# Kernel optimization log

Measured on AMD Instinct MI355X. Metric: run time of the kernel, lower is better.

The kernel has to match this reference:

```python
import jax, jax.numpy as jnp
import numpy as np

B, S, D, H, F = 2, 2048, 2048, 16, 6144
HD = D // H  # 128
EPS = 1e-5
NEG = -1e9


def layernorm(x, g, b):
    m = jnp.mean(x, axis=-1, keepdims=True)
    v = jnp.var(x, axis=-1, keepdims=True)
    return (x - m) * jax.lax.rsqrt(v + EPS) * g + b


def setup_inputs() -> dict:
    key = jax.random.key(0)
    ks = jax.random.split(key, 16)
    w = 0.02
    hidden_states = jax.random.normal(ks[0], (B, S, D), jnp.float32)
    # additive causal mask [B,1,S,S]
    causal = jnp.tril(jnp.ones((S, S), jnp.bool_))
    attention_mask = jnp.broadcast_to(jnp.where(causal, 0.0, NEG).astype(jnp.float32)[None, None], (B, 1, S, S))
    # ALiBi position bias [H,S,S]
    slopes = 2.0 ** (-8.0 * (jnp.arange(1, H + 1, dtype=jnp.float32)) / H)
    rel = (jnp.arange(S)[None, :] - jnp.arange(S)[:, None]).astype(jnp.float32)  # j - i (<=0 causal)
    position_bias = slopes[:, None, None] * rel[None]
    params = dict(
        ln1_g=jnp.ones((D,), jnp.float32), ln1_b=jnp.zeros((D,), jnp.float32),
        w_qkv=jax.random.normal(ks[1], (D, 3 * D), jnp.float32) * w,
        b_qkv=jnp.zeros((3 * D,), jnp.float32),
        w_o=jax.random.normal(ks[2], (D, D), jnp.float32) * w,
        b_o=jnp.zeros((D,), jnp.float32),
        ln2_g=jnp.ones((D,), jnp.float32), ln2_b=jnp.zeros((D,), jnp.float32),
        w_fc=jax.random.normal(ks[3], (D, F), jnp.float32) * w,
        b_fc=jnp.zeros((F,), jnp.float32),
        w_fc2=jax.random.normal(ks[4], (D, F), jnp.float32) * w,
        b_fc2=jnp.zeros((F,), jnp.float32),
        w_proj=jax.random.normal(ks[5], (F, D), jnp.float32) * w,
        b_proj=jnp.zeros((D,), jnp.float32),
    )
    return dict(hidden_states=hidden_states, attention_mask=attention_mask,
                position_bias=position_bias, **params)


def reference(hidden_states, attention_mask, position_bias,
              ln1_g, ln1_b, w_qkv, b_qkv, w_o, b_o,
              ln2_g, ln2_b, w_fc, b_fc, w_fc2, b_fc2, w_proj, b_proj):
    residual = hidden_states
    h = layernorm(hidden_states, ln1_g, ln1_b)
    qkv = h @ w_qkv + b_qkv  # [B,S,3D]
    q, k, v = jnp.split(qkv, 3, axis=-1)
    # split heads -> [B,H,S,HD]
    def heads(t):
        return t.reshape(B, S, H, HD).transpose(0, 2, 1, 3)
    q, k, v = heads(q), heads(k), heads(v)
    # muP scaling: attn_scale_power=1.0 -> divide by head_dim
    scores = jnp.einsum('bhqd,bhkd->bhqk', q, k) / jnp.float32(HD)
    scores = scores + attention_mask + position_bias[None]
    probs = jax.nn.softmax(scores, axis=-1)
    ctx = jnp.einsum('bhqk,bhkd->bhqd', probs, v)
    ctx = ctx.transpose(0, 2, 1, 3).reshape(B, S, D)
    attn_out = ctx @ w_o + b_o
    hidden = attn_out + residual
    # SwiGLU MLP
    residual = hidden
    h2 = layernorm(hidden, ln2_g, ln2_b)
    gate = h2 @ w_fc2 + b_fc2
    up = h2 @ w_fc + b_fc
    mlp = (up * jax.nn.silu(gate)) @ w_proj + b_proj
    return mlp + residual
```

## Files before the change

kernel.cpp:

```cpp
#include <hip/hip_runtime.h>
#include <hip/hip_bf16.h>
#include <math.h>

#define DI __device__ __forceinline__

typedef __bf16 bf16x8 __attribute__((ext_vector_type(8)));
typedef float f32x4 __attribute__((ext_vector_type(4)));
typedef short s16x8 __attribute__((ext_vector_type(8)));

DI unsigned short f2bf(float f) {
  unsigned int u = __builtin_bit_cast(unsigned int, f);
  unsigned int r = (u + 0x7fffu + ((u >> 16) & 1u)) >> 16;
  return (unsigned short)r;
}
DI float bf2f(unsigned short h) {
  unsigned int u = ((unsigned int)h) << 16;
  return __builtin_bit_cast(float, u);
}

DI void gload16(const void* g, void* l) {
  __builtin_amdgcn_global_load_lds(
      (const __attribute__((address_space(1))) void*)g,
      (__attribute__((address_space(3))) void*)l, 16, 0, 0);
}

DI unsigned ldsoff(const void* p) {
  return (unsigned)(size_t)(const __attribute__((address_space(3))) void*)p;
}

template <int OFF>
DI bf16x8 ds128(unsigned base) {
  bf16x8 r;
  asm volatile("ds_read_b128 %0, %1 offset:%2" : "=v"(r) : "v"(base), "i"(OFF));
  return r;
}
template <int N>
DI void lgkm() {
  asm volatile("s_waitcnt lgkmcnt(%0)" ::"i"(N));
  __builtin_amdgcn_sched_barrier(0);
}
template <int N>
DI void vmc() {
  asm volatile("s_waitcnt vmcnt(%0)" ::"i"(N));
  __builtin_amdgcn_sched_barrier(0);
}

DI void xcd_map(int BN, int& m0, int& n0) {
  const int nx = gridDim.x;
  int orig = blockIdx.y * nx + blockIdx.x;
  int xcd = orig & 7, k = orig >> 3;
  int xm = xcd >> 2, xn = xcd & 3;
  int nband = nx >> 2;
  m0 = (xm * 8 + (k & 7)) * 256;
  n0 = (xn * nband + (k >> 3)) * BN;
}

__global__ __launch_bounds__(256)
void transpose_cast_f32(const float* __restrict__ in, unsigned short* __restrict__ out,
                        int R, int C) {
  __shared__ unsigned int t[64 * 65];
  const int r0 = blockIdx.y * 64, c0 = blockIdx.x * 64;
  const int tid = threadIdx.x;
#pragma unroll
  for (int p = 0; p < 4; ++p) {
    int e = p * 1024 + tid * 4;
    int r = e >> 6, c = e & 63;
    float4 v = *(const float4*)(in + (size_t)(r0 + r) * C + c0 + c);
    t[r * 65 + c + 0] = f2bf(v.x);
    t[r * 65 + c + 1] = f2bf(v.y);
    t[r * 65 + c + 2] = f2bf(v.z);
    t[r * 65 + c + 3] = f2bf(v.w);
  }
  __syncthreads();
  const int oc = tid >> 2, ch = tid & 3;
  alignas(16) unsigned short vals[16];
#pragma unroll
  for (int j = 0; j < 16; ++j) vals[j] = (unsigned short)t[(ch * 16 + j) * 65 + oc];
  size_t ob = (size_t)(c0 + oc) * R + r0 + ch * 16;
  *(s16x8*)(out + ob) = *(const s16x8*)(vals);
  *(s16x8*)(out + ob + 8) = *(const s16x8*)(vals + 8);
}

__global__ __launch_bounds__(256)
void transpose_v(const unsigned short* __restrict__ qkv, unsigned short* __restrict__ vT) {
  __shared__ unsigned int t[64 * 65];
  const int s0 = blockIdx.x * 64, d0 = blockIdx.y * 64, bh = blockIdx.z;
  const int b = bh >> 4, h = bh & 15;
  const int tid = threadIdx.x;
#pragma unroll
  for (int p = 0; p < 2; ++p) {
    int id = p * 256 + tid;
    int r = id >> 3, c = (id & 7) * 8;
    s16x8 v = *(const s16x8*)(qkv + (size_t)(b * 2048 + s0 + r) * 6144 + 4096 + h * 128 + d0 + c);
#pragma unroll
    for (int j = 0; j < 8; ++j) t[r * 65 + c + j] = (unsigned short)((const unsigned short*)&v)[j];
  }
  __syncthreads();
  const int oc = tid >> 2, ch = tid & 3;
  alignas(16) unsigned short vals[16];
#pragma unroll
  for (int j = 0; j < 16; ++j) vals[j] = (unsigned short)t[(ch * 16 + j) * 65 + oc];
  size_t ob = (size_t)(bh * 128 + d0 + oc) * 2048 + s0 + ch * 16;
  *(s16x8*)(vT + ob) = *(const s16x8*)(vals);
  *(s16x8*)(vT + ob + 8) = *(const s16x8*)(vals + 8);
}

__global__ __launch_bounds__(256)
void ln_kernel(const float* __restrict__ x, const float* __restrict__ g,
               const float* __restrict__ bi, unsigned short* __restrict__ y) {
  __shared__ float red[8];
  const int row = blockIdx.x, tid = threadIdx.x;
  const float* xp = x + (size_t)row * 2048 + tid * 8;
  float4 v0 = *(const float4*)xp;
  float4 v1 = *(const float4*)(xp + 4);
  float v[8] = {v0.x, v0.y, v0.z, v0.w, v1.x, v1.y, v1.z, v1.w};
  float s = 0.f;
#pragma unroll
  for (int j = 0; j < 8; ++j) s += v[j];
#pragma unroll
  for (int d = 1; d < 64; d <<= 1) s += __shfl_xor(s, d);
  if ((tid & 63) == 0) red[tid >> 6] = s;
  __syncthreads();
  float mean = (red[0] + red[1] + red[2] + red[3]) * (1.f / 2048.f);
  float dd[8], sq = 0.f;
#pragma unroll
  for (int j = 0; j < 8; ++j) { dd[j] = v[j] - mean; sq += dd[j] * dd[j]; }
#pragma unroll
  for (int d = 1; d < 64; d <<= 1) sq += __shfl_xor(sq, d);
  if ((tid & 63) == 0) red[4 + (tid >> 6)] = sq;
  __syncthreads();
  float var = (red[4] + red[5] + red[6] + red[7]) * (1.f / 2048.f);
  float rs = rsqrtf(var + 1e-5f);
  float4 g0 = *(const float4*)(g + tid * 8), g1 = *(const float4*)(g + tid * 8 + 4);
  float4 b0 = *(const float4*)(bi + tid * 8), b1 = *(const float4*)(bi + tid * 8 + 4);
  float gg[8] = {g0.x, g0.y, g0.z, g0.w, g1.x, g1.y, g1.z, g1.w};
  float bb[8] = {b0.x, b0.y, b0.z, b0.w, b1.x, b1.y, b1.z, b1.w};
  alignas(16) unsigned short o[8];
#pragma unroll
  for (int j = 0; j < 8; ++j) o[j] = f2bf(dd[j] * rs * gg[j] + bb[j]);
  *(s16x8*)(y + (size_t)row * 2048 + tid * 8) = *(const s16x8*)o;
}

DI void stage_half(const unsigned short* __restrict__ G, int ld, int rbase, int kt,
                   int h, unsigned short* dst, int tid) {
#pragma unroll
  for (int i = 0; i < 2; ++i) {
    int id = i * 512 + tid;
    int rl = id >> 3, sl = id & 7;
    int ss = sl ^ (rl & 7);
    gload16(G + (size_t)(rbase + h * 128 + rl) * ld + kt + ss * 8,
            (char*)dst + h * 16384 + id * 16);
  }
}

template <int MODE>
__global__ __launch_bounds__(512, 2)
void gemm256(const unsigned short* __restrict__ A, int lda,
             const unsigned short* __restrict__ B,
             const float* __restrict__ bias,
             const void* __restrict__ resg,
             void* __restrict__ out, int ldc, int K) {
  __shared__ alignas(16) unsigned short As[2][256 * 64];
  __shared__ alignas(16) unsigned short Bs[2][256 * 64];

  const int tid = threadIdx.x;
  const int l = tid & 63, w = tid >> 6;
  const int wr = w >> 2, wc = w & 3;
  const int lr = l & 15, lg = l >> 4;

  int m0, n0;
  xcd_map(256, m0, n0);

  const int NT = K >> 6;

  f32x4 acc[8][4];
  const f32x4 z4 = {0.f, 0.f, 0.f, 0.f};
#pragma unroll
  for (int i = 0; i < 8; ++i)
#pragma unroll
    for (int j = 0; j < 4; ++j) acc[i][j] = z4;

  const int s7 = lr & 7;
  const unsigned swz0 = (unsigned)((lg ^ s7) << 4);
  const unsigned swz1 = (unsigned)(((4 | lg) ^ s7) << 4);
  const unsigned rA = (unsigned)((wr * 128 + lr) * 128);
  const unsigned rB = (unsigned)((wc * 64 + lr) * 128);
  const unsigned aA0 = ldsoff(&As[0][0]) + rA + swz0;
  const unsigned aA1 = ldsoff(&As[0][0]) + rA + swz1;
  const unsigned bA0 = ldsoff(&Bs[0][0]) + rB + swz0;
  const unsigned bA1 = ldsoff(&Bs[0][0]) + rB + swz1;

  stage_half(A, lda, m0, 0, 0, As[0], tid);
  stage_half(A, lda, m0, 0, 1, As[0], tid);
  stage_half(B, K, n0, 0, 0, Bs[0], tid);
  stage_half(B, K, n0, 0, 1, Bs[0], tid);
  if (NT > 1) {
    stage_half(B, K, n0, 64, 0, Bs[1], tid);
    stage_half(B, K, n0, 64, 1, Bs[1], tid);
    stage_half(A, lda, m0, 64, 0, As[1], tid);
    asm volatile("s_waitcnt vmcnt(6)" ::: "memory");
  } else {
    asm volatile("s_waitcnt vmcnt(0)" ::: "memory");
  }
  __builtin_amdgcn_s_barrier();

  for (int t = 0; t < NT; ++t) {
    const unsigned co = (unsigned)((t & 1) * 32768);
    const unsigned a0b = aA0 + co, a1b = aA1 + co;
    const unsigned b0b = bA0 + co, b1b = bA1 + co;
    bf16x8 a0[4][2], a1[4][2], bfr[4][2];

#pragma unroll
    for (int i = 0; i < 4; ++i) {
      a0[i][0] = ds128<0 * 2048>(a0b + i * 2048);
      a0[i][1] = ds128<0 * 2048>(a1b + i * 2048);
    }
#pragma unroll
    for (int j = 0; j < 2; ++j) {
      bfr[j][0] = ds128<0>(b0b + j * 2048);
      bfr[j][1] = ds128<0>(b1b + j * 2048);
    }
    if (t + 1 < NT) stage_half(A, lda, m0, (t + 1) * 64, 1, As[(t & 1) ^ 1], tid);
#pragma unroll
    for (int j = 2; j < 4; ++j) {
      bfr[j][0] = ds128<0>(b0b + j * 2048);
      bfr[j][1] = ds128<0>(b1b + j * 2048);
    }
    lgkm<4>();
    __builtin_amdgcn_s_setprio(1);
#pragma unroll
    for (int i = 0; i < 4; ++i)
#pragma unroll
      for (int j = 0; j < 2; ++j)
#pragma unroll
        for (int kk = 0; kk < 2; ++kk)
          acc[i][j] = __builtin_amdgcn_mfma_f32_16x16x32_bf16(a0[i][kk], bfr[j][kk], acc[i][j], 0, 0, 0);
    __builtin_amdgcn_s_setprio(0);
    __builtin_amdgcn_s_barrier();

#pragma unroll
    for (int i = 0; i < 4; ++i) {
      a1[i][0] = ds128<8192>(a0b + i * 2048);
      a1[i][1] = ds128<8192>(a1b + i * 2048);
    }
    lgkm<8>();
    __builtin_amdgcn_s_setprio(1);
#pragma unroll
    for (int i = 0; i < 4; ++i)
#pragma unroll
      for (int j = 2; j < 4; ++j)
#pragma unroll
        for (int kk = 0; kk < 2; ++kk)
          acc[i][j] = __builtin_amdgcn_mfma_f32_16x16x32_bf16(a0[i][kk], bfr[j][kk], acc[i][j], 0, 0, 0);
    __builtin_amdgcn_s_setprio(0);
    __builtin_amdgcn_s_barrier();

    if (t + 2 < NT) stage_half(B, K, n0, (t + 2) * 64, 0, Bs[t & 1], tid);
    lgkm<0>();
    __builtin_amdgcn_s_setprio(1);
#pragma unroll
    for (int i = 0; i < 4; ++i)
#pragma unroll
      for (int j = 0; j < 2; ++j)
#pragma unroll
        for (int kk = 0; kk < 2; ++kk)
          acc[i + 4][j] = __builtin_amdgcn_mfma_f32_16x16x32_bf16(a1[i][kk], bfr[j][kk], acc[i + 4][j], 0, 0, 0);
    __builtin_amdgcn_s_setprio(0);
    __builtin_amdgcn_s_barrier();

    if (t + 2 < NT) {
      stage_half(B, K, n0, (t + 2) * 64, 1, Bs[t & 1], tid);
      stage_half(A, lda, m0, (t + 2) * 64, 0, As[t & 1], tid);
    }
    __builtin_amdgcn_s_setprio(1);
#pragma unroll
    for (int i = 0; i < 4; ++i)
#pragma unroll
      for (int j = 2; j < 4; ++j)
#pragma unroll
        for (int kk = 0; kk < 2; ++kk)
          acc[i + 4][j] = __builtin_amdgcn_mfma_f32_16x16x32_bf16(a1[i][kk], bfr[j][kk], acc[i + 4][j], 0, 0, 0);
    __builtin_amdgcn_s_setprio(0);
    if (t + 2 < NT) { vmc<6>(); } else { vmc<0>(); }
    __builtin_amdgcn_s_barrier();
  }

#pragma unroll
  for (int i = 0; i < 8; ++i) {
    int r0 = m0 + wr * 128 + i * 16 + lg * 4;
#pragma unroll
    for (int j = 0; j < 4; ++j) {
      int col = n0 + wc * 64 + j * 16 + lr;
      float bb = bias[col];
#pragma unroll
      for (int q = 0; q < 4; ++q) {
        size_t off = (size_t)(r0 + q) * ldc + col;
        float v = acc[i][j][q] + bb;
        if (MODE == 0) {
          ((unsigned short*)out)[off] = f2bf(v);
        } else {
          ((float*)out)[off] = v + ((const float*)resg)[off];
        }
      }
    }
  }
}

template <int MODE, bool DUAL>
__global__ __launch_bounds__(512, 2)
void gemm_n128(const unsigned short* __restrict__ A, int lda,
               const unsigned short* __restrict__ B0,
               const unsigned short* __restrict__ B1,
               const float* __restrict__ bias0, const float* __restrict__ bias1,
               const void* __restrict__ resg,
               void* __restrict__ out, int ldc, int K) {
  __shared__ alignas(16) unsigned short As[2][256 * 64];
  __shared__ alignas(16) unsigned short Bs0[2][128 * 64];

  const int tid = threadIdx.x;
  const int l = tid & 63, w = tid >> 6;
  const int wr = w >> 2, wc = w & 3;
  const int lr = l & 15, lg = l >> 4;

  int m0, n0;
  xcd_map(128, m0, n0);

  const int NT = K >> 6;

  f32x4 acc0[8][2];
  const f32x4 z4 = {0.f, 0.f, 0.f, 0.f};
#pragma unroll
  for (int i = 0; i < 8; ++i)
#pragma unroll
    for (int j = 0; j < 2; ++j) acc0[i][j] = z4;

  const int s7 = lr & 7;
  const unsigned swz0 = (unsigned)((lg ^ s7) << 4);
  const unsigned swz1 = (unsigned)(((4 | lg) ^ s7) << 4);
  const unsigned rA = (unsigned)((wr * 128 + lr) * 128);
  const unsigned rB = (unsigned)((wc * 32 + lr) * 128);
  const unsigned aA0 = ldsoff(&As[0][0]) + rA + swz0;
  const unsigned aA1 = ldsoff(&As[0][0]) + rA + swz1;
  const unsigned bA0 = ldsoff(&Bs0[0][0]) + rB + swz0;
  const unsigned bA1 = ldsoff(&Bs0[0][0]) + rB + swz1;

  stage_half(A, lda, m0, 0, 0, As[0], tid);
  stage_half(A, lda, m0, 0, 1, As[0], tid);
  stage_half(B0, K, n0, 0, 0, Bs0[0], tid);
  if (NT > 1) {
    stage_half(B0, K, n0, 64, 0, Bs0[1], tid);
    stage_half(A, lda, m0, 64, 0, As[1], tid);
    asm volatile("s_waitcnt vmcnt(4)" ::: "memory");
  } else {
    asm volatile("s_waitcnt vmcnt(0)" ::: "memory");
  }
  __builtin_amdgcn_s_barrier();

  for (int t = 0; t < NT; ++t) {
    const int cur = t & 1;
    const unsigned ca = aA0 + (unsigned)(cur * 32768);
    const unsigned ca1 = aA1 + (unsigned)(cur * 32768);
    const unsigned cb = bA0 + (unsigned)(cur * 16384);
    const unsigned cb1 = bA1 + (unsigned)(cur * 16384);
    bf16x8 a0[4][2], a1[4][2], b0f[2][2];

#pragma unroll
    for (int i = 0; i < 4; ++i) {
      a0[i][0] = ds128<0>(ca + i * 2048);
      a0[i][1] = ds128<0>(ca1 + i * 2048);
    }
#pragma unroll
    for (int j = 0; j < 2; ++j) {
      b0f[j][0] = ds128<0>(cb + j * 2048);
      b0f[j][1] = ds128<0>(cb1 + j * 2048);
    }
    if (t + 1 < NT) stage_half(A, lda, m0, (t + 1) * 64, 1, As[cur ^ 1], tid);
#pragma unroll
    for (int i = 0; i < 4; ++i) {
      a1[i][0] = ds128<8192>(ca + i * 2048);
      a1[i][1] = ds128<8192>(ca1 + i * 2048);
    }
    lgkm<8>();
    __builtin_amdgcn_s_setprio(1);
#pragma unroll
    for (int i = 0; i < 4; ++i)
#pragma unroll
      for (int j = 0; j < 2; ++j)
#pragma unroll
        for (int kk = 0; kk < 2; ++kk)
          acc0[i][j] = __builtin_amdgcn_mfma_f32_16x16x32_bf16(a0[i][kk], b0f[j][kk], acc0[i][j], 0, 0, 0);
    __builtin_amdgcn_s_setprio(0);
    __builtin_amdgcn_s_barrier();

    if (t + 2 < NT) stage_half(B0, K, n0, (t + 2) * 64, 0, Bs0[cur], tid);
    lgkm<0>();
    if (t + 2 < NT) stage_half(A, lda, m0, (t + 2) * 64, 0, As[cur], tid);
    __builtin_amdgcn_s_setprio(1);
#pragma unroll
    for (int i = 0; i < 4; ++i)
#pragma unroll
      for (int j = 0; j < 2; ++j)
#pragma unroll
        for (int kk = 0; kk < 2; ++kk)
          acc0[i + 4][j] = __builtin_amdgcn_mfma_f32_16x16x32_bf16(a1[i][kk], b0f[j][kk], acc0[i + 4][j], 0, 0, 0);
    __builtin_amdgcn_s_setprio(0);
    if (t + 2 < NT) { vmc<4>(); } else { vmc<0>(); }
    __builtin_amdgcn_s_barrier();
  }

#pragma unroll
  for (int i = 0; i < 8; ++i) {
    int r0 = m0 + wr * 128 + i * 16 + lg * 4;
#pragma unroll
    for (int j = 0; j < 2; ++j) {
      int col = n0 + wc * 32 + j * 16 + lr;
      float bb0 = bias0[col];
#pragma unroll
      for (int q = 0; q < 4; ++q) {
        size_t off = (size_t)(r0 + q) * ldc + col;
        float v = acc0[i][j][q] + bb0;
        ((float*)out)[off] = v + ((const float*)resg)[off];
      }
    }
  }
}

DI void mmq(f32x4 (&acc)[8][2], int io, const bf16x8 (&af)[4][2], const bf16x8 (&bf)[2][2]) {
#pragma unroll
  for (int kk = 0; kk < 2; ++kk)
#pragma unroll
    for (int i = 0; i < 4; ++i)
#pragma unroll
      for (int j = 0; j < 2; ++j)
        acc[io + i][j] = __builtin_amdgcn_mfma_f32_16x16x32_bf16(af[i][kk], bf[j][kk], acc[io + i][j], 0, 0, 0);
}

#define RDA(dst, B0_, B1_, OFS)                                        \
  dst[0][0] = ds128<(OFS) + 0>(B0_);    dst[0][1] = ds128<(OFS) + 0>(B1_);    \
  dst[1][0] = ds128<(OFS) + 2048>(B0_); dst[1][1] = ds128<(OFS) + 2048>(B1_); \
  dst[2][0] = ds128<(OFS) + 4096>(B0_); dst[2][1] = ds128<(OFS) + 4096>(B1_); \
  dst[3][0] = ds128<(OFS) + 6144>(B0_); dst[3][1] = ds128<(OFS) + 6144>(B1_);

#define RDB(dst, B0_, B1_, OFS)                                        \
  dst[0][0] = ds128<(OFS) + 0>(B0_);    dst[0][1] = ds128<(OFS) + 0>(B1_);    \
  dst[1][0] = ds128<(OFS) + 2048>(B0_); dst[1][1] = ds128<(OFS) + 2048>(B1_);

#define MLP_ITER(t, CUR, A0C, B0C, B1C, A1C, A0N, B0N)                         \
  {                                                                            \
               \
    RDB(B1C, cA0, cA1, (CUR) * 16384);                                         \
    lgkm<4>();                                                                 \
    __builtin_amdgcn_s_setprio(1);                                             \
    mmq(acc0, 0, A0C, B0C);                                                    \
    __builtin_amdgcn_s_setprio(0);                                             \
    __builtin_amdgcn_sched_barrier(0);                                         \
    __builtin_amdgcn_s_barrier();                                              \
      \
    if ((t) + 2 < NT) stage_half(B0, K, n0, ((t) + 2) * 64, 0, Bs0[CUR], tid); \
    RDA(A1C, aA0, aA1, (CUR) * 32768 + 8192);                                  \
    lgkm<8>();                                                                 \
    __builtin_amdgcn_s_setprio(1);                                             \
    mmq(acc1, 0, A0C, B1C);                                                    \
    __builtin_amdgcn_s_setprio(0);                                             \
    if ((t) + 2 < NT) { vmc<2>(); } else { vmc<0>(); }                         \
    __builtin_amdgcn_s_barrier();                                              \
    \
    if ((t) + 2 < NT) stage_half(B1, K, n0, ((t) + 2) * 64, 0, Bs1[CUR], tid); \
    RDA(A0N, aA0, aA1, ((CUR) ^ 1) * 32768);                                   \
    lgkm<8>();                                                                 \
    __builtin_amdgcn_s_setprio(1);                                             \
    mmq(acc0, 4, A1C, B0C);                                                    \
    __builtin_amdgcn_s_setprio(0);                                             \
    __builtin_amdgcn_sched_barrier(0);                                         \
    __builtin_amdgcn_s_barrier();                                              \
     \
    if ((t) + 2 < NT) {                                                        \
      stage_half(A, lda, m0, ((t) + 2) * 64, 0, As[CUR], tid);                 \
      stage_half(A, lda, m0, ((t) + 2) * 64, 1, As[CUR], tid);                 \
    }                                                                          \
    RDB(B0N, bA0, bA1, ((CUR) ^ 1) * 16384);                                   \
    __builtin_amdgcn_sched_barrier(0);                                         \
    __builtin_amdgcn_s_setprio(1);                                             \
    mmq(acc1, 4, A1C, B1C);                                                    \
    __builtin_amdgcn_s_setprio(0);                                             \
    __builtin_amdgcn_sched_barrier(0);                                         \
    __builtin_amdgcn_s_barrier();                                              \
  }

__global__ __launch_bounds__(512, 2)
void gemm_mlp(const unsigned short* __restrict__ A, int lda,
              const unsigned short* __restrict__ B0,
              const unsigned short* __restrict__ B1,
              const float* __restrict__ bias0, const float* __restrict__ bias1,
              unsigned short* __restrict__ out, int ldc, int K) {
  __shared__ alignas(16) unsigned short As[2][256 * 64];
  __shared__ alignas(16) unsigned short Bs0[2][128 * 64];
  __shared__ alignas(16) unsigned short Bs1[2][128 * 64];

  const int tid = threadIdx.x;
  const int l = tid & 63, w = tid >> 6;
  const int wr = w >> 2, wc = w & 3;
  const int lr = l & 15, lg = l >> 4;

  int m0, n0;
  xcd_map(128, m0, n0);
  const int NT = K >> 6;

  f32x4 acc0[8][2], acc1[8][2];
  const f32x4 z4 = {0.f, 0.f, 0.f, 0.f};
#pragma unroll
  for (int i = 0; i < 8; ++i)
#pragma unroll
    for (int j = 0; j < 2; ++j) { acc0[i][j] = z4; acc1[i][j] = z4; }

  const int s7 = lr & 7;
  const unsigned swz0 = (unsigned)((lg ^ s7) << 4);
  const unsigned swz1 = (unsigned)(((4 | lg) ^ s7) << 4);
  const unsigned rA = (unsigned)((wr * 128 + lr) * 128);
  const unsigned rB = (unsigned)((wc * 32 + lr) * 128);
  const unsigned aA0 = ldsoff(&As[0][0]) + rA + swz0;
  const unsigned aA1 = ldsoff(&As[0][0]) + rA + swz1;
  const unsigned bA0 = ldsoff(&Bs0[0][0]) + rB + swz0;
  const unsigned bA1 = ldsoff(&Bs0[0][0]) + rB + swz1;
  const unsigned cA0 = ldsoff(&Bs1[0][0]) + rB + swz0;
  const unsigned cA1 = ldsoff(&Bs1[0][0]) + rB + swz1;

  bf16x8 a0X[4][2], a1X[4][2], b0X[2][2], b1X[2][2];
  bf16x8 a0Y[4][2], a1Y[4][2], b0Y[2][2], b1Y[2][2];

  stage_half(A, lda, m0, 0, 0, As[0], tid);
  stage_half(A, lda, m0, 0, 1, As[0], tid);
  stage_half(B0, K, n0, 0, 0, Bs0[0], tid);
  stage_half(B1, K, n0, 0, 0, Bs1[0], tid);
  stage_half(B0, K, n0, 64, 0, Bs0[1], tid);
  stage_half(B1, K, n0, 64, 0, Bs1[1], tid);
  stage_half(A, lda, m0, 64, 0, As[1], tid);
  stage_half(A, lda, m0, 64, 1, As[1], tid);
  vmc<8>();
  __builtin_amdgcn_s_barrier();
  RDA(a0X, aA0, aA1, 0);
  RDB(b0X, bA0, bA1, 0);

  for (int t = 0; t < NT; t += 2) {
    MLP_ITER(t, 0, a0X, b0X, b1X, a1X, a0Y, b0Y);
    MLP_ITER(t + 1, 1, a0Y, b0Y, b1Y, a1Y, a0X, b0X);
  }

#pragma unroll
  for (int i = 0; i < 8; ++i) {
    int r0 = m0 + wr * 128 + i * 16 + lg * 4;
#pragma unroll
    for (int j = 0; j < 2; ++j) {
      int col = n0 + wc * 32 + j * 16 + lr;
      float bb0 = bias0[col];
      float bb1 = bias1[col];
#pragma unroll
      for (int q = 0; q < 4; ++q) {
        size_t off = (size_t)(r0 + q) * ldc + col;
        float v = acc0[i][j][q] + bb0;
        float gt = acc1[i][j][q] + bb1;
        out[off] = f2bf(v * (gt / (1.f + expf(-gt))));
      }
    }
  }
}

__global__ __launch_bounds__(256, 2)
void attn_kernel(const unsigned short* __restrict__ qkv,
                 const unsigned short* __restrict__ vT,
                 unsigned short* __restrict__ ctx) {
  __shared__ unsigned short Ks[64 * 128];
  __shared__ unsigned short Vs[128 * 64];
  __shared__ unsigned short Ps[4][16 * 80];
  __shared__ unsigned short Ob[4][16 * 136];

  const int g = blockIdx.x;
  const int xcd = g & 7, slot = g >> 3;
  const int bh = xcd * 4 + (slot & 3);
  const int pid = slot >> 2;
  const int b = bh >> 4, h = bh & 15;
  const int tid = threadIdx.x, l = tid & 63, w = tid >> 6;
  const int lr = l & 15, lg = l >> 4;
  const float slope2 = exp2f(-0.5f * (float)(h + 1)) * 1.44269504f;
  const float SC2 = 0.0078125f * 1.44269504f;

  const int krow = tid >> 4, kcb = tid & 15;
  const int vrow = tid >> 3, vcb = tid & 7;
  const unsigned short* kbase = qkv + (size_t)(b * 2048 + krow) * 6144 + 2048 + h * 128 + kcb * 8;
  const unsigned short* vbase = vT + (size_t)(bh * 128 + vrow) * 2048 + vcb * 8;
  char* kdst = (char*)Ks + krow * 256 + ((kcb ^ (krow & 7)) << 4);
  char* vdst = (char*)Vs + vrow * 128 + ((vcb ^ (vrow & 7)) << 4);

  int4 kr[4], vr[4];
#pragma unroll
  for (int p = 0; p < 4; ++p) {
    kr[p] = *(const int4*)(kbase + (size_t)p * 16 * 6144);
    vr[p] = *(const int4*)(vbase + (size_t)p * 32 * 2048);
  }

  for (int tq = 0; tq < 2; ++tq) {
    const int qb = tq ? (31 - pid) : pid;
    const int q0 = qb * 64;
    bf16x8 aq[4];
    {
      const unsigned short* qp =
          qkv + (size_t)(b * 2048 + q0 + w * 16 + lr) * 6144 + h * 128 + lg * 8;
#pragma unroll
      for (int kk = 0; kk < 4; ++kk) aq[kk] = *(const bf16x8*)(qp + kk * 32);
    }
    const f32x4 z4 = {0.f, 0.f, 0.f, 0.f};
    f32x4 acc[8];
#pragma unroll
    for (int dt = 0; dt < 8; ++dt) acc[dt] = z4;
    float m_r[4] = {-INFINITY, -INFINITY, -INFINITY, -INFINITY};
    float l_r[4] = {0.f, 0.f, 0.f, 0.f};
    const int ibase = q0 + w * 16 + lg * 4;
    const int nc = qb + 1;

    for (int c = 0; c < nc; ++c) {
      const int kv0 = c * 64;
      __syncthreads();
#pragma unroll
      for (int p = 0; p < 4; ++p) {
        *(int4*)(kdst + p * 4096) = kr[p];
        *(int4*)(vdst + p * 4096) = vr[p];
      }
      __syncthreads();
      {
        int nxt = (c + 1 < nc) ? (c + 1) * 64 : (tq == 0 ? 0 : -1);
        if (nxt >= 0) {
#pragma unroll
          for (int p = 0; p < 4; ++p) {
            kr[p] = *(const int4*)(kbase + (size_t)nxt * 6144 + (size_t)p * 16 * 6144);
            vr[p] = *(const int4*)(vbase + nxt + (size_t)p * 32 * 2048);
          }
        }
      }

      f32x4 sc[4];
#pragma unroll
      for (int t = 0; t < 4; ++t) sc[t] = z4;
      __builtin_amdgcn_s_setprio(1);
#pragma unroll
      for (int t = 0; t < 4; ++t) {
#pragma unroll
        for (int kk = 0; kk < 4; ++kk) {
          int row = t * 16 + lr;
          int bo = (row * 256 + kk * 64 + lg * 16) ^ ((row & 7) << 4);
          bf16x8 bk = *(const bf16x8*)((const char*)Ks + bo);
          sc[t] = __builtin_amdgcn_mfma_f32_16x16x32_bf16(aq[kk], bk, sc[t], 0, 0, 0);
        }
      }
      __builtin_amdgcn_s_setprio(0);
      float cmax[4] = {-INFINITY, -INFINITY, -INFINITY, -INFINITY};
#pragma unroll
      for (int t = 0; t < 4; ++t)
#pragma unroll
        for (int q = 0; q < 4; ++q) {
          int j = kv0 + t * 16 + lr;
          int i = ibase + q;
          float s = sc[t][q] * SC2 + slope2 * (float)(j - i);
          if (j > i) s = -1e9f;
          sc[t][q] = s;
          cmax[q] = fmaxf(cmax[q], s);
        }
#pragma unroll
      for (int q = 0; q < 4; ++q) {
        float v = cmax[q];
        v = fmaxf(v, __shfl_xor(v, 1));
        v = fmaxf(v, __shfl_xor(v, 2));
        v = fmaxf(v, __shfl_xor(v, 4));
        v = fmaxf(v, __shfl_xor(v, 8));
        cmax[q] = v;
      }
      float alpha[4], rsum[4];
#pragma unroll
      for (int q = 0; q < 4; ++q) {
        float mn = fmaxf(m_r[q], cmax[q]);
        alpha[q] = exp2f(m_r[q] - mn);
        m_r[q] = mn;
        rsum[q] = 0.f;
      }
#pragma unroll
      for (int t = 0; t < 4; ++t)
#pragma unroll
        for (int q = 0; q < 4; ++q) {
          float p = exp2f(sc[t][q] - m_r[q]);
          rsum[q] += p;
          sc[t][q] = p;
        }
#pragma unroll
      for (int q = 0; q < 4; ++q) {
        float v = rsum[q];
        v += __shfl_xor(v, 1);
        v += __shfl_xor(v, 2);
        v += __shfl_xor(v, 4);
        v += __shfl_xor(v, 8);
        l_r[q] = l_r[q] * alpha[q] + v;
      }
#pragma unroll
      for (int dt = 0; dt < 8; ++dt)
#pragma unroll
        for (int q = 0; q < 4; ++q) acc[dt][q] *= alpha[q];
#pragma unroll
      for (int t = 0; t < 4; ++t)
#pragma unroll
        for (int q = 0; q < 4; ++q)
          Ps[w][(lg * 4 + q) * 80 + t * 16 + lr] = f2bf(sc[t][q]);
      __builtin_amdgcn_s_setprio(1);
#pragma unroll
      for (int kc = 0; kc < 2; ++kc) {
        bf16x8 ap = *(const bf16x8*)(&Ps[w][lr * 80 + kc * 32 + lg * 8]);
#pragma unroll
        for (int dt = 0; dt < 8; ++dt) {
          int row = dt * 16 + lr;
          int bo = (row * 128 + kc * 64 + lg * 16) ^ ((row & 7) << 4);
          bf16x8 bv = *(const bf16x8*)((const char*)Vs + bo);
          acc[dt] = __builtin_amdgcn_mfma_f32_16x16x32_bf16(ap, bv, acc[dt], 0, 0, 0);
        }
      }
      __builtin_amdgcn_s_setprio(0);
    }

    unsigned short* Kw = &Ob[w][0];
#pragma unroll
    for (int q = 0; q < 4; ++q) {
      float inv = 1.f / l_r[q];
      int rl = lg * 4 + q;
#pragma unroll
      for (int dt = 0; dt < 8; ++dt)
        Kw[rl * 136 + dt * 16 + lr] = f2bf(acc[dt][q] * inv);
    }
    const int rr = l >> 2, c4 = l & 3;
    const unsigned short* srow = Kw + rr * 136 + c4 * 8;
    size_t gb = (size_t)(b * 2048 + q0 + w * 16 + rr) * 2048 + h * 128 + c4 * 8;
#pragma unroll
    for (int k = 0; k < 4; ++k)
      *(s16x8*)(ctx + gb + k * 32) = *(const s16x8*)(srow + k * 32);
  }
}

extern "C" void kernel_launch(void* const* d_in, const int* in_sizes, int n_in,
                              void* d_out, int out_size, void* d_ws, size_t ws_size,
                              hipStream_t stream) {
  const float* hs   = (const float*)d_in[0];
  const float* ln1g = (const float*)d_in[3];
  const float* ln1b = (const float*)d_in[4];
  const float* wqkv = (const float*)d_in[5];
  const float* bqkv = (const float*)d_in[6];
  const float* wo   = (const float*)d_in[7];
  const float* bo   = (const float*)d_in[8];
  const float* ln2g = (const float*)d_in[9];
  const float* ln2b = (const float*)d_in[10];
  const float* wfc  = (const float*)d_in[11];
  const float* bfc  = (const float*)d_in[12];
  const float* wfc2 = (const float*)d_in[13];
  const float* bfc2 = (const float*)d_in[14];
  const float* wpj  = (const float*)d_in[15];
  const float* bpj  = (const float*)d_in[16];

  char* ws = (char*)d_ws;
  unsigned short* woT   = (unsigned short*)(ws + 0);
  unsigned short* wfcT  = (unsigned short*)(ws + 8388608);
  unsigned short* wfc2T = (unsigned short*)(ws + 33554432);
  unsigned short* hbuf  = (unsigned short*)(ws + 58720256);
  unsigned short* qkvb  = (unsigned short*)(ws + 75497472);
  unsigned short* wqkvT = (unsigned short*)(ws + 125829120);
  unsigned short* vTb   = (unsigned short*)(ws + 150994944);
  unsigned short* ctxb  = (unsigned short*)(ws + 167772160);
  unsigned short* wpjT  = wqkvT;
  float* outf = (float*)d_out;

  dim3 blk(256), blk512(512);
  transpose_cast_f32<<<dim3(96, 32), blk, 0, stream>>>(wqkv, wqkvT, 2048, 6144);
  transpose_cast_f32<<<dim3(32, 32), blk, 0, stream>>>(wo, woT, 2048, 2048);
  transpose_cast_f32<<<dim3(96, 32), blk, 0, stream>>>(wfc, wfcT, 2048, 6144);
  transpose_cast_f32<<<dim3(96, 32), blk, 0, stream>>>(wfc2, wfc2T, 2048, 6144);
  ln_kernel<<<dim3(4096), blk, 0, stream>>>(hs, ln1g, ln1b, hbuf);
  gemm256<0><<<dim3(24, 16), blk512, 0, stream>>>(hbuf, 2048, wqkvT, bqkv, nullptr,
                                                  qkvb, 6144, 2048);
  transpose_v<<<dim3(32, 2, 32), blk, 0, stream>>>(qkvb, vTb);
  transpose_cast_f32<<<dim3(32, 96), blk, 0, stream>>>(wpj, wpjT, 6144, 2048);
  attn_kernel<<<dim3(512), blk, 0, stream>>>(qkvb, vTb, ctxb);
  gemm_n128<1, false><<<dim3(16, 16), blk512, 0, stream>>>(
      ctxb, 2048, woT, nullptr, bo, nullptr, hs, d_out, 2048, 2048);
  ln_kernel<<<dim3(4096), blk, 0, stream>>>(outf, ln2g, ln2b, hbuf);
  gemm_mlp<<<dim3(48, 16), blk512, 0, stream>>>(
      hbuf, 2048, wfcT, wfc2T, bfc, bfc2, qkvb, 6144, 2048);
  gemm_n128<1, false><<<dim3(16, 16), blk512, 0, stream>>>(
      qkvb, 6144, wpjT, nullptr, bpj, nullptr, outf, d_out, 2048, 6144);
}
```

Baseline: 690.2 us.

## Restructure GEMM main loops to a simpler ping-pong schedule with extra barriers

Both the generic 256x256 GEMM and the fused SwiGLU MLP GEMM get a reworked per-K-tile schedule. The MLP kernel drops its register double-buffered MLP_ITER macro, which prefetched the next tile's fragments across iterations, in favour of a plain loop that reads fragments for the current tile only. Additional s_barriers are placed around the LDS reads, apparently to keep waves in lockstep in a ping-pong pattern. Global staging is regrouped into whole-tile chunks with adjusted vmcnt waits. This gives up cross-iteration register prefetch and adds synchronisation points, in exchange for lower register pressure and more regular wave coordination.

New measurement: 701.0 us. Within noise of the previous version (+1.6%).

```diff
diff --git a/kernel.cpp b/kernel.cpp
--- a/kernel.cpp
+++ b/kernel.cpp
@@ -153,6 +153,16 @@
   }
 }
 
+#define RDA(dst, B0_, B1_, OFS)                                        \
+  dst[0][0] = ds128<(OFS) + 0>(B0_);    dst[0][1] = ds128<(OFS) + 0>(B1_);    \
+  dst[1][0] = ds128<(OFS) + 2048>(B0_); dst[1][1] = ds128<(OFS) + 2048>(B1_); \
+  dst[2][0] = ds128<(OFS) + 4096>(B0_); dst[2][1] = ds128<(OFS) + 4096>(B1_); \
+  dst[3][0] = ds128<(OFS) + 6144>(B0_); dst[3][1] = ds128<(OFS) + 6144>(B1_);
+
+#define RDB(dst, B0_, B1_, OFS)                                        \
+  dst[0][0] = ds128<(OFS) + 0>(B0_);    dst[0][1] = ds128<(OFS) + 0>(B1_);    \
+  dst[1][0] = ds128<(OFS) + 2048>(B0_); dst[1][1] = ds128<(OFS) + 2048>(B1_);
+
 template <int MODE>
 __global__ __launch_bounds__(512, 2)
 void gemm256(const unsigned short* __restrict__ A, int lda,
@@ -194,39 +204,25 @@
   stage_half(A, lda, m0, 0, 1, As[0], tid);
   stage_half(B, K, n0, 0, 0, Bs[0], tid);
   stage_half(B, K, n0, 0, 1, Bs[0], tid);
-  if (NT > 1) {
-    stage_half(B, K, n0, 64, 0, Bs[1], tid);
-    stage_half(B, K, n0, 64, 1, Bs[1], tid);
-    stage_half(A, lda, m0, 64, 0, As[1], tid);
-    asm volatile("s_waitcnt vmcnt(6)" ::: "memory");
-  } else {
-    asm volatile("s_waitcnt vmcnt(0)" ::: "memory");
-  }
+  stage_half(B, K, n0, 64, 0, Bs[1], tid);
+  stage_half(B, K, n0, 64, 1, Bs[1], tid);
+  stage_half(A, lda, m0, 64, 0, As[1], tid);
+  stage_half(A, lda, m0, 64, 1, As[1], tid);
+  vmc<8>();
   __builtin_amdgcn_s_barrier();
 
   for (int t = 0; t < NT; ++t) {
     const unsigned co = (unsigned)((t & 1) * 32768);
-    const unsigned a0b = aA0 + co, a1b = aA1 + co;
-    const unsigned b0b = bA0 + co, b1b = bA1 + co;
+    const unsigned pA0 = aA0 + co, pA1 = aA1 + co;
+    const unsigned pB0 = bA0 + co, pB1 = bA1 + co;
     bf16x8 a0[4][2], a1[4][2], bfr[4][2];
 
-#pragma unroll
-    for (int i = 0; i < 4; ++i) {
-      a0[i][0] = ds128<0 * 2048>(a0b + i * 2048);
-      a0[i][1] = ds128<0 * 2048>(a1b + i * 2048);
-    }
-#pragma unroll
-    for (int j = 0; j < 2; ++j) {
-      bfr[j][0] = ds128<0>(b0b + j * 2048);
-      bfr[j][1] = ds128<0>(b1b + j * 2048);
-    }
-    if (t + 1 < NT) stage_half(A, lda, m0, (t + 1) * 64, 1, As[(t & 1) ^ 1], tid);
-#pragma unroll
-    for (int j = 2; j < 4; ++j) {
-      bfr[j][0] = ds128<0>(b0b + j * 2048);
-      bfr[j][1] = ds128<0>(b1b + j * 2048);
-    }
-    lgkm<4>();
+    RDA(a0, pA0, pA1, 0);
+    bfr[0][0] = ds128<0>(pB0);    bfr[0][1] = ds128<0>(pB1);
+    bfr[1][0] = ds128<2048>(pB0); bfr[1][1] = ds128<2048>(pB1);
+    lgkm<8>();
+    __builtin_amdgcn_s_barrier();
+    lgkm<0>();
     __builtin_amdgcn_s_setprio(1);
 #pragma unroll
     for (int i = 0; i < 4; ++i)
@@ -238,12 +234,10 @@
     __builtin_amdgcn_s_setprio(0);
     __builtin_amdgcn_s_barrier();
 
-#pragma unroll
-    for (int i = 0; i < 4; ++i) {
-      a1[i][0] = ds128<8192>(a0b + i * 2048);
-      a1[i][1] = ds128<8192>(a1b + i * 2048);
-    }
-    lgkm<8>();
+    bfr[2][0] = ds128<4096>(pB0); bfr[2][1] = ds128<4096>(pB1);
+    bfr[3][0] = ds128<6144>(pB0); bfr[3][1] = ds128<6144>(pB1);
+    __builtin_amdgcn_s_barrier();
+    lgkm<0>();
     __builtin_amdgcn_s_setprio(1);
 #pragma unroll
     for (int i = 0; i < 4; ++i)
@@ -255,7 +249,12 @@
     __builtin_amdgcn_s_setprio(0);
     __builtin_amdgcn_s_barrier();
 
-    if (t + 2 < NT) stage_half(B, K, n0, (t + 2) * 64, 0, Bs[t & 1], tid);
+    RDA(a1, pA0, pA1, 8192);
+    if (t + 2 < NT) {
+      stage_half(B, K, n0, (t + 2) * 64, 0, Bs[t & 1], tid);
+      stage_half(B, K, n0, (t + 2) * 64, 1, Bs[t & 1], tid);
+    }
+    __builtin_amdgcn_s_barrier();
     lgkm<0>();
     __builtin_amdgcn_s_setprio(1);
 #pragma unroll
@@ -269,9 +268,10 @@
     __builtin_amdgcn_s_barrier();
 
     if (t + 2 < NT) {
-      stage_half(B, K, n0, (t + 2) * 64, 1, Bs[t & 1], tid);
       stage_half(A, lda, m0, (t + 2) * 64, 0, As[t & 1], tid);
-    }
+      stage_half(A, lda, m0, (t + 2) * 64, 1, As[t & 1], tid);
+    }
+    __builtin_amdgcn_sched_barrier(0);
     __builtin_amdgcn_s_setprio(1);
 #pragma unroll
     for (int i = 0; i < 4; ++i)
@@ -281,7 +281,7 @@
         for (int kk = 0; kk < 2; ++kk)
           acc[i + 4][j] = __builtin_amdgcn_mfma_f32_16x16x32_bf16(a1[i][kk], bfr[j][kk], acc[i + 4][j], 0, 0, 0);
     __builtin_amdgcn_s_setprio(0);
-    if (t + 2 < NT) { vmc<6>(); } else { vmc<0>(); }
+    if (t + 2 < NT) { vmc<8>(); } else { vmc<0>(); }
     __builtin_amdgcn_s_barrier();
   }
 
@@ -434,58 +434,6 @@
       for (int j = 0; j < 2; ++j)
         acc[io + i][j] = __builtin_amdgcn_mfma_f32_16x16x32_bf16(af[i][kk], bf[j][kk], acc[io + i][j], 0, 0, 0);
 }
-
-#define RDA(dst, B0_, B1_, OFS)                                        \
-  dst[0][0] = ds128<(OFS) + 0>(B0_);    dst[0][1] = ds128<(OFS) + 0>(B1_);    \
-  dst[1][0] = ds128<(OFS) + 2048>(B0_); dst[1][1] = ds128<(OFS) + 2048>(B1_); \
-  dst[2][0] = ds128<(OFS) + 4096>(B0_); dst[2][1] = ds128<(OFS) + 4096>(B1_); \
-  dst[3][0] = ds128<(OFS) + 6144>(B0_); dst[3][1] = ds128<(OFS) + 6144>(B1_);
-
-#define RDB(dst, B0_, B1_, OFS)                                        \
-  dst[0][0] = ds128<(OFS) + 0>(B0_);    dst[0][1] = ds128<(OFS) + 0>(B1_);    \
-  dst[1][0] = ds128<(OFS) + 2048>(B0_); dst[1][1] = ds128<(OFS) + 2048>(B1_);
-
-#define MLP_ITER(t, CUR, A0C, B0C, B1C, A1C, A0N, B0N)                         \
-  {                                                                            \
-               \
-    RDB(B1C, cA0, cA1, (CUR) * 16384);                                         \
-    lgkm<4>();                                                                 \
-    __builtin_amdgcn_s_setprio(1);                                             \
-    mmq(acc0, 0, A0C, B0C);                                                    \
-    __builtin_amdgcn_s_setprio(0);                                             \
-    __builtin_amdgcn_sched_barrier(0);                                         \
-    __builtin_amdgcn_s_barrier();                                              \
-      \
-    if ((t) + 2 < NT) stage_half(B0, K, n0, ((t) + 2) * 64, 0, Bs0[CUR], tid); \
-    RDA(A1C, aA0, aA1, (CUR) * 32768 + 8192);                                  \
-    lgkm<8>();                                                                 \
-    __builtin_amdgcn_s_setprio(1);                                             \
-    mmq(acc1, 0, A0C, B1C);                                                    \
-    __builtin_amdgcn_s_setprio(0);                                             \
-    if ((t) + 2 < NT) { vmc<2>(); } else { vmc<0>(); }                         \
-    __builtin_amdgcn_s_barrier();                                              \
-    \
-    if ((t) + 2 < NT) stage_half(B1, K, n0, ((t) + 2) * 64, 0, Bs1[CUR], tid); \
-    RDA(A0N, aA0, aA1, ((CUR) ^ 1) * 32768);                                   \
-    lgkm<8>();                                                                 \
-    __builtin_amdgcn_s_setprio(1);                                             \
-    mmq(acc0, 4, A1C, B0C);                                                    \
-    __builtin_amdgcn_s_setprio(0);                                             \
-    __builtin_amdgcn_sched_barrier(0);                                         \
-    __builtin_amdgcn_s_barrier();                                              \
-     \
-    if ((t) + 2 < NT) {                                                        \
-      stage_half(A, lda, m0, ((t) + 2) * 64, 0, As[CUR], tid);                 \
-      stage_half(A, lda, m0, ((t) + 2) * 64, 1, As[CUR], tid);                 \
-    }                                                                          \
-    RDB(B0N, bA0, bA1, ((CUR) ^ 1) * 16384);                                   \
-    __builtin_amdgcn_sched_barrier(0);                                         \
-    __builtin_amdgcn_s_setprio(1);                                             \
-    mmq(acc1, 4, A1C, B1C);                                                    \
-    __builtin_amdgcn_s_setprio(0);                                             \
-    __builtin_amdgcn_sched_barrier(0);                                         \
-    __builtin_amdgcn_s_barrier();                                              \
-  }
 
 __global__ __launch_bounds__(512, 2)
 void gemm_mlp(const unsigned short* __restrict__ A, int lda,
@@ -525,9 +473,6 @@
   const unsigned cA0 = ldsoff(&Bs1[0][0]) + rB + swz0;
   const unsigned cA1 = ldsoff(&Bs1[0][0]) + rB + swz1;
 
-  bf16x8 a0X[4][2], a1X[4][2], b0X[2][2], b1X[2][2];
-  bf16x8 a0Y[4][2], a1Y[4][2], b0Y[2][2], b1Y[2][2];
-
   stage_half(A, lda, m0, 0, 0, As[0], tid);
   stage_half(A, lda, m0, 0, 1, As[0], tid);
   stage_half(B0, K, n0, 0, 0, Bs0[0], tid);
@@ -538,12 +483,53 @@
   stage_half(A, lda, m0, 64, 1, As[1], tid);
   vmc<8>();
   __builtin_amdgcn_s_barrier();
-  RDA(a0X, aA0, aA1, 0);
-  RDB(b0X, bA0, bA1, 0);
-
-  for (int t = 0; t < NT; t += 2) {
-    MLP_ITER(t, 0, a0X, b0X, b1X, a1X, a0Y, b0Y);
-    MLP_ITER(t + 1, 1, a0Y, b0Y, b1Y, a1Y, a0X, b0X);
+
+  for (int t = 0; t < NT; ++t) {
+    const unsigned coA = (unsigned)((t & 1) * 32768);
+    const unsigned coB = (unsigned)((t & 1) * 16384);
+    const unsigned pA0 = aA0 + coA, pA1 = aA1 + coA;
+    const unsigned pB0 = bA0 + coB, pB1 = bA1 + coB;
+    const unsigned pC0 = cA0 + coB, pC1 = cA1 + coB;
+    bf16x8 a0[4][2], a1[4][2], b0f[2][2], b1f[2][2];
+
+    RDA(a0, pA0, pA1, 0);
+    RDB(b0f, pB0, pB1, 0);
+    lgkm<8>();
+    __builtin_amdgcn_s_barrier();
+    lgkm<0>();
+    __builtin_amdgcn_s_setprio(1);
+    mmq(acc0, 0, a0, b0f);
+    __builtin_amdgcn_s_setprio(0);
+    __builtin_amdgcn_s_barrier();
+
+    RDB(b1f, pC0, pC1, 0);
+    if (t + 2 < NT) stage_half(B0, K, n0, (t + 2) * 64, 0, Bs0[t & 1], tid);
+    __builtin_amdgcn_s_barrier();
+    lgkm<0>();
+    __builtin_amdgcn_s_setprio(1);
+    mmq(acc1, 0, a0, b1f);
+    __builtin_amdgcn_s_setprio(0);
+    __builtin_amdgcn_s_barrier();
+
+    RDA(a1, pA0, pA1, 8192);
+    if (t + 2 < NT) stage_half(B1, K, n0, (t + 2) * 64, 0, Bs1[t & 1], tid);
+    __builtin_amdgcn_s_barrier();
+    lgkm<0>();
+    __builtin_amdgcn_s_setprio(1);
+    mmq(acc0, 4, a1, b0f);
+    __builtin_amdgcn_s_setprio(0);
+    __builtin_amdgcn_s_barrier();
+
+    if (t + 2 < NT) {
+      stage_half(A, lda, m0, (t + 2) * 64, 0, As[t & 1], tid);
+      stage_half(A, lda, m0, (t + 2) * 64, 1, As[t & 1], tid);
+    }
+    __builtin_amdgcn_sched_barrier(0);
+    __builtin_amdgcn_s_setprio(1);
+    mmq(acc1, 4, a1, b1f);
+    __builtin_amdgcn_s_setprio(0);
+    if (t + 2 < NT) { vmc<8>(); } else { vmc<0>(); }
+    __builtin_amdgcn_s_barrier();
   }
 
 #pragma unroll
```

## Give each attention block one query tile and drop output staging buffer

Applied to the files above, without the earlier changes.

The attention kernel previously paired two query tiles per block (pid and 31-pid) to balance causal work. Now each of 1024 blocks handles one query tile, scheduled longest-first (qb = 31 - slot/4). The Ob output buffer is removed and the epilogue reuses the Ps buffer in two halves, cutting LDS so launch bounds can ask for 3 blocks per SM. This trades the explicit pairing balance for more parallelism and occupancy, and relies on the hardware scheduler to even out the uneven per-block work.

After: 723.6 us. 4.8% more time.

```diff
diff --git a/kernel.cpp b/kernel.cpp
--- a/kernel.cpp
+++ b/kernel.cpp
@@ -152,6 +152,16 @@
             (char*)dst + h * 16384 + id * 16);
   }
 }
+
+#define RDA(dst, B0_, B1_, OFS)                                        \
+  dst[0][0] = ds128<(OFS) + 0>(B0_);    dst[0][1] = ds128<(OFS) + 0>(B1_);    \
+  dst[1][0] = ds128<(OFS) + 2048>(B0_); dst[1][1] = ds128<(OFS) + 2048>(B1_); \
+  dst[2][0] = ds128<(OFS) + 4096>(B0_); dst[2][1] = ds128<(OFS) + 4096>(B1_); \
+  dst[3][0] = ds128<(OFS) + 6144>(B0_); dst[3][1] = ds128<(OFS) + 6144>(B1_);
+
+#define RDB(dst, B0_, B1_, OFS)                                        \
+  dst[0][0] = ds128<(OFS) + 0>(B0_);    dst[0][1] = ds128<(OFS) + 0>(B1_);    \
+  dst[1][0] = ds128<(OFS) + 2048>(B0_); dst[1][1] = ds128<(OFS) + 2048>(B1_);
 
 template <int MODE>
 __global__ __launch_bounds__(512, 2)
@@ -212,8 +222,8 @@
 
 #pragma unroll
     for (int i = 0; i < 4; ++i) {
-      a0[i][0] = ds128<0 * 2048>(a0b + i * 2048);
-      a0[i][1] = ds128<0 * 2048>(a1b + i * 2048);
+      a0[i][0] = ds128<0>(a0b + i * 2048);
+      a0[i][1] = ds128<0>(a1b + i * 2048);
     }
 #pragma unroll
     for (int j = 0; j < 2; ++j) {
@@ -434,16 +444,6 @@
       for (int j = 0; j < 2; ++j)
         acc[io + i][j] = __builtin_amdgcn_mfma_f32_16x16x32_bf16(af[i][kk], bf[j][kk], acc[io + i][j], 0, 0, 0);
 }
-
-#define RDA(dst, B0_, B1_, OFS)                                        \
-  dst[0][0] = ds128<(OFS) + 0>(B0_);    dst[0][1] = ds128<(OFS) + 0>(B1_);    \
-  dst[1][0] = ds128<(OFS) + 2048>(B0_); dst[1][1] = ds128<(OFS) + 2048>(B1_); \
-  dst[2][0] = ds128<(OFS) + 4096>(B0_); dst[2][1] = ds128<(OFS) + 4096>(B1_); \
-  dst[3][0] = ds128<(OFS) + 6144>(B0_); dst[3][1] = ds128<(OFS) + 6144>(B1_);
-
-#define RDB(dst, B0_, B1_, OFS)                                        \
-  dst[0][0] = ds128<(OFS) + 0>(B0_);    dst[0][1] = ds128<(OFS) + 0>(B1_);    \
-  dst[1][0] = ds128<(OFS) + 2048>(B0_); dst[1][1] = ds128<(OFS) + 2048>(B1_);
 
 #define MLP_ITER(t, CUR, A0C, B0C, B1C, A1C, A0N, B0N)                         \
   {                                                                            \
@@ -565,19 +565,18 @@
   }
 }
 
-__global__ __launch_bounds__(256, 2)
+__global__ __launch_bounds__(256, 3)
 void attn_kernel(const unsigned short* __restrict__ qkv,
                  const unsigned short* __restrict__ vT,
                  unsigned short* __restrict__ ctx) {
   __shared__ unsigned short Ks[64 * 128];
   __shared__ unsigned short Vs[128 * 64];
   __shared__ unsigned short Ps[4][16 * 80];
-  __shared__ unsigned short Ob[4][16 * 136];
 
   const int g = blockIdx.x;
   const int xcd = g & 7, slot = g >> 3;
   const int bh = xcd * 4 + (slot & 3);
-  const int pid = slot >> 2;
+  const int qb = 31 - (slot >> 2);
   const int b = bh >> 4, h = bh & 15;
   const int tid = threadIdx.x, l = tid & 63, w = tid >> 6;
   const int lr = l & 15, lg = l >> 4;
@@ -598,145 +597,143 @@
     vr[p] = *(const int4*)(vbase + (size_t)p * 32 * 2048);
   }
 
-  for (int tq = 0; tq < 2; ++tq) {
-    const int qb = tq ? (31 - pid) : pid;
-    const int q0 = qb * 64;
-    bf16x8 aq[4];
-    {
-      const unsigned short* qp =
-          qkv + (size_t)(b * 2048 + q0 + w * 16 + lr) * 6144 + h * 128 + lg * 8;
-#pragma unroll
-      for (int kk = 0; kk < 4; ++kk) aq[kk] = *(const bf16x8*)(qp + kk * 32);
-    }
-    const f32x4 z4 = {0.f, 0.f, 0.f, 0.f};
-    f32x4 acc[8];
-#pragma unroll
-    for (int dt = 0; dt < 8; ++dt) acc[dt] = z4;
-    float m_r[4] = {-INFINITY, -INFINITY, -INFINITY, -INFINITY};
-    float l_r[4] = {0.f, 0.f, 0.f, 0.f};
-    const int ibase = q0 + w * 16 + lg * 4;
-    const int nc = qb + 1;
-
-    for (int c = 0; c < nc; ++c) {
-      const int kv0 = c * 64;
-      __syncthreads();
+  const int q0 = qb * 64;
+  bf16x8 aq[4];
+  {
+    const unsigned short* qp =
+        qkv + (size_t)(b * 2048 + q0 + w * 16 + lr) * 6144 + h * 128 + lg * 8;
+#pragma unroll
+    for (int kk = 0; kk < 4; ++kk) aq[kk] = *(const bf16x8*)(qp + kk * 32);
+  }
+  const f32x4 z4 = {0.f, 0.f, 0.f, 0.f};
+  f32x4 acc[8];
+#pragma unroll
+  for (int dt = 0; dt < 8; ++dt) acc[dt] = z4;
+  float m_r[4] = {-INFINITY, -INFINITY, -INFINITY, -INFINITY};
+  float l_r[4] = {0.f, 0.f, 0.f, 0.f};
+  const int ibase = q0 + w * 16 + lg * 4;
+  const int nc = qb + 1;
+
+  for (int c = 0; c < nc; ++c) {
+    const int kv0 = c * 64;
+    __syncthreads();
+#pragma unroll
+    for (int p = 0; p < 4; ++p) {
+      *(int4*)(kdst + p * 4096) = kr[p];
+      *(int4*)(vdst + p * 4096) = vr[p];
+    }
+    __syncthreads();
+    if (c + 1 < nc) {
+      int nxt = (c + 1) * 64;
 #pragma unroll
       for (int p = 0; p < 4; ++p) {
-        *(int4*)(kdst + p * 4096) = kr[p];
-        *(int4*)(vdst + p * 4096) = vr[p];
+        kr[p] = *(const int4*)(kbase + (size_t)nxt * 6144 + (size_t)p * 16 * 6144);
+        vr[p] = *(const int4*)(vbase + nxt + (size_t)p * 32 * 2048);
       }
-      __syncthreads();
-      {
-        int nxt = (c + 1 < nc) ? (c + 1) * 64 : (tq == 0 ? 0 : -1);
-        if (nxt >= 0) {
-#pragma unroll
-          for (int p = 0; p < 4; ++p) {
-            kr[p] = *(const int4*)(kbase + (size_t)nxt * 6144 + (size_t)p * 16 * 6144);
-            vr[p] = *(const int4*)(vbase + nxt + (size_t)p * 32 * 2048);
-          }
-        }
+    }
+
+    f32x4 sc[4];
+#pragma unroll
+    for (int t = 0; t < 4; ++t) sc[t] = z4;
+    __builtin_amdgcn_s_setprio(1);
+#pragma unroll
+    for (int t = 0; t < 4; ++t) {
+#pragma unroll
+      for (int kk = 0; kk < 4; ++kk) {
+        int row = t * 16 + lr;
+        int bo = (row * 256 + kk * 64 + lg * 16) ^ ((row & 7) << 4);
+        bf16x8 bk = *(const bf16x8*)((const char*)Ks + bo);
+        sc[t] = __builtin_amdgcn_mfma_f32_16x16x32_bf16(aq[kk], bk, sc[t], 0, 0, 0);
       }
-
-      f32x4 sc[4];
-#pragma unroll
-      for (int t = 0; t < 4; ++t) sc[t] = z4;
-      __builtin_amdgcn_s_setprio(1);
-#pragma unroll
-      for (int t = 0; t < 4; ++t) {
-#pragma unroll
-        for (int kk = 0; kk < 4; ++kk) {
-          int row = t * 16 + lr;
-          int bo = (row * 256 + kk * 64 + lg * 16) ^ ((row & 7) << 4);
-          bf16x8 bk = *(const bf16x8*)((const char*)Ks + bo);
-          sc[t] = __builtin_amdgcn_mfma_f32_16x16x32_bf16(aq[kk], bk, sc[t], 0, 0, 0);
-        }
+    }
+    __builtin_amdgcn_s_setprio(0);
+    float cmax[4] = {-INFINITY, -INFINITY, -INFINITY, -INFINITY};
+#pragma unroll
+    for (int t = 0; t < 4; ++t)
+#pragma unroll
+      for (int q = 0; q < 4; ++q) {
+        int j = kv0 + t * 16 + lr;
+        int i = ibase + q;
+        float s = sc[t][q] * SC2 + slope2 * (float)(j - i);
+        if (j > i) s = -1e9f;
+        sc[t][q] = s;
+        cmax[q] = fmaxf(cmax[q], s);
       }
-      __builtin_amdgcn_s_setprio(0);
-      float cmax[4] = {-INFINITY, -INFINITY, -INFINITY, -INFINITY};
-#pragma unroll
-      for (int t = 0; t < 4; ++t)
-#pragma unroll
-        for (int q = 0; q < 4; ++q) {
-          int j = kv0 + t * 16 + lr;
-          int i = ibase + q;
-          float s = sc[t][q] * SC2 + slope2 * (float)(j - i);
-          if (j > i) s = -1e9f;
-          sc[t][q] = s;
-          cmax[q] = fmaxf(cmax[q], s);
-        }
+#pragma unroll
+    for (int q = 0; q < 4; ++q) {
+      float v = cmax[q];
+      v = fmaxf(v, __shfl_xor(v, 1));
+      v = fmaxf(v, __shfl_xor(v, 2));
+      v = fmaxf(v, __shfl_xor(v, 4));
+      v = fmaxf(v, __shfl_xor(v, 8));
+      cmax[q] = v;
+    }
+    float alpha[4], rsum[4];
+#pragma unroll
+    for (int q = 0; q < 4; ++q) {
+      float mn = fmaxf(m_r[q], cmax[q]);
+      alpha[q] = exp2f(m_r[q] - mn);
+      m_r[q] = mn;
+      rsum[q] = 0.f;
+    }
+#pragma unroll
+    for (int t = 0; t < 4; ++t)
 #pragma unroll
       for (int q = 0; q < 4; ++q) {
-        float v = cmax[q];
-        v = fmaxf(v, __shfl_xor(v, 1));
-        v = fmaxf(v, __shfl_xor(v, 2));
-        v = fmaxf(v, __shfl_xor(v, 4));
-        v = fmaxf(v, __shfl_xor(v, 8));
-        cmax[q] = v;
+        float p = exp2f(sc[t][q] - m_r[q]);
+        rsum[q] += p;
+        sc[t][q] = p;
       }
-      float alpha[4], rsum[4];
-#pragma unroll
-      for (int q = 0; q < 4; ++q) {
-        float mn = fmaxf(m_r[q], cmax[q]);
-        alpha[q] = exp2f(m_r[q] - mn);
-        m_r[q] = mn;
-        rsum[q] = 0.f;
+#pragma unroll
+    for (int q = 0; q < 4; ++q) {
+      float v = rsum[q];
+      v += __shfl_xor(v, 1);
+      v += __shfl_xor(v, 2);
+      v += __shfl_xor(v, 4);
+      v += __shfl_xor(v, 8);
+      l_r[q] = l_r[q] * alpha[q] + v;
+    }
+#pragma unroll
+    for (int dt = 0; dt < 8; ++dt)
+#pragma unroll
+      for (int q = 0; q < 4; ++q) acc[dt][q] *= alpha[q];
+#pragma unroll
+    for (int t = 0; t < 4; ++t)
+#pragma unroll
+      for (int q = 0; q < 4; ++q)
+        Ps[w][(lg * 4 + q) * 80 + t * 16 + lr] = f2bf(sc[t][q]);
+    __builtin_amdgcn_s_setprio(1);
+#pragma unroll
+    for (int kc = 0; kc < 2; ++kc) {
+      bf16x8 ap = *(const bf16x8*)(&Ps[w][lr * 80 + kc * 32 + lg * 8]);
+#pragma unroll
+      for (int dt = 0; dt < 8; ++dt) {
+        int row = dt * 16 + lr;
+        int bo = (row * 128 + kc * 64 + lg * 16) ^ ((row & 7) << 4);
+        bf16x8 bv = *(const bf16x8*)((const char*)Vs + bo);
+        acc[dt] = __builtin_amdgcn_mfma_f32_16x16x32_bf16(ap, bv, acc[dt], 0, 0, 0);
       }
-#pragma unroll
-      for (int t = 0; t < 4; ++t)
-#pragma unroll
-        for (int q = 0; q < 4; ++q) {
-          float p = exp2f(sc[t][q] - m_r[q]);
-          rsum[q] += p;
-          sc[t][q] = p;
-        }
-#pragma unroll
-      for (int q = 0; q < 4; ++q) {
-        float v = rsum[q];
-        v += __shfl_xor(v, 1);
-        v += __shfl_xor(v, 2);
-        v += __shfl_xor(v, 4);
-        v += __shfl_xor(v, 8);
-        l_r[q] = l_r[q] * alpha[q] + v;
-      }
-#pragma unroll
-      for (int dt = 0; dt < 8; ++dt)
-#pragma unroll
-        for (int q = 0; q < 4; ++q) acc[dt][q] *= alpha[q];
-#pragma unroll
-      for (int t = 0; t < 4; ++t)
-#pragma unroll
-        for (int q = 0; q < 4; ++q)
-          Ps[w][(lg * 4 + q) * 80 + t * 16 + lr] = f2bf(sc[t][q]);
-      __builtin_amdgcn_s_setprio(1);
-#pragma unroll
-      for (int kc = 0; kc < 2; ++kc) {
-        bf16x8 ap = *(const bf16x8*)(&Ps[w][lr * 80 + kc * 32 + lg * 8]);
-#pragma unroll
-        for (int dt = 0; dt < 8; ++dt) {
-          int row = dt * 16 + lr;
-          int bo = (row * 128 + kc * 64 + lg * 16) ^ ((row & 7) << 4);
-          bf16x8 bv = *(const bf16x8*)((const char*)Vs + bo);
-          acc[dt] = __builtin_amdgcn_mfma_f32_16x16x32_bf16(ap, bv, acc[dt], 0, 0, 0);
-        }
-      }
-      __builtin_amdgcn_s_setprio(0);
-    }
-
-    unsigned short* Kw = &Ob[w][0];
+    }
+    __builtin_amdgcn_s_setprio(0);
+  }
+
+  float inv4[4];
+#pragma unroll
+  for (int q = 0; q < 4; ++q) inv4[q] = 1.f / l_r[q];
+  const int rr = l >> 2, c4 = l & 3;
+#pragma unroll
+  for (int chv = 0; chv < 2; ++chv) {
 #pragma unroll
     for (int q = 0; q < 4; ++q) {
-      float inv = 1.f / l_r[q];
       int rl = lg * 4 + q;
 #pragma unroll
-      for (int dt = 0; dt < 8; ++dt)
-        Kw[rl * 136 + dt * 16 + lr] = f2bf(acc[dt][q] * inv);
-    }
-    const int rr = l >> 2, c4 = l & 3;
-    const unsigned short* srow = Kw + rr * 136 + c4 * 8;
-    size_t gb = (size_t)(b * 2048 + q0 + w * 16 + rr) * 2048 + h * 128 + c4 * 8;
-#pragma unroll
-    for (int k = 0; k < 4; ++k)
-      *(s16x8*)(ctx + gb + k * 32) = *(const s16x8*)(srow + k * 32);
+      for (int dt = 0; dt < 4; ++dt)
+        Ps[w][rl * 80 + dt * 16 + lr] = f2bf(acc[chv * 4 + dt][q] * inv4[q]);
+    }
+    const unsigned short* srow = &Ps[w][rr * 80 + c4 * 8];
+    size_t gb = (size_t)(b * 2048 + q0 + w * 16 + rr) * 2048 + h * 128 + chv * 64 + c4 * 8;
+    *(s16x8*)(ctx + gb) = *(const s16x8*)(srow);
+    *(s16x8*)(ctx + gb + 32) = *(const s16x8*)(srow + 32);
   }
 }
 
@@ -781,7 +778,7 @@
                                                   qkvb, 6144, 2048);
   transpose_v<<<dim3(32, 2, 32), blk, 0, stream>>>(qkvb, vTb);
   transpose_cast_f32<<<dim3(32, 96), blk, 0, stream>>>(wpj, wpjT, 6144, 2048);
-  attn_kernel<<<dim3(512), blk, 0, stream>>>(qkvb, vTb, ctxb);
+  attn_kernel<<<dim3(1024), blk, 0, stream>>>(qkvb, vTb, ctxb);
   gemm_n128<1, false><<<dim3(16, 16), blk512, 0, stream>>>(
       ctxb, 2048, woT, nullptr, bo, nullptr, hs, d_out, 2048, 2048);
   ln_kernel<<<dim3(4096), blk, 0, stream>>>(outf, ln2g, ln2b, hbuf);
```
